# Performance work log

Hardware: AMD Instinct MI355X
Metric: run time of the kernel (lower is better)

## Reference

```python
import jax, jax.numpy as jnp
import numpy as np

B, C, H, W = 16, 16, 256, 256
HID, OUT_C, IN_C = 128, 13, 3

_SOBEL_X = np.array([[-1, 0, 1], [-2, 0, 2], [-1, 0, 1]], dtype=np.float32)
_SOBEL_Y = _SOBEL_X.T


def setup_inputs() -> dict:
    key = jax.random.key(0)
    k1, k2, k3, k4 = jax.random.split(key, 4)
    return {
        "input_grid": jax.random.normal(k1, (B, C, H, W), dtype=jnp.float32),
        "w1": jax.random.normal(k2, (HID, 3 * C), dtype=jnp.float32) * 0.0001,
        "b1": jax.random.normal(k3, (HID,), dtype=jnp.float32) * 0.0001,
        "w2": jax.random.normal(k4, (OUT_C, HID), dtype=jnp.float32) * 0.0001,
    }


def _depthwise_sobel(x_padded, filt2d):
    # x_padded: [B, C, H+2, W+2]; depthwise 3x3 valid conv (groups=C)
    c = x_padded.shape[1]
    kern = jnp.broadcast_to(jnp.asarray(filt2d)[None, None], (c, 1, 3, 3))
    return jax.lax.conv_general_dilated(
        x_padded, kern, window_strides=(1, 1), padding="VALID",
        feature_group_count=c,
        dimension_numbers=("NCHW", "OIHW", "NCHW"))


def reference(input_grid, w1, b1, w2):
    # circular pad by 1 on spatial dims
    xp = jnp.pad(input_grid, ((0, 0), (0, 0), (1, 1), (1, 1)), mode="wrap")
    gx = _depthwise_sobel(xp, _SOBEL_X)
    gy = _depthwise_sobel(xp, _SOBEL_Y)
    # perception grid: [B, 3C, H, W]
    perception = jnp.concatenate([input_grid, gx, gy], axis=1)
    # update network: 1x1 conv -> ReLU -> 1x1 conv (dropout = identity in eval)
    h = jax.nn.relu(jnp.einsum("bchw,oc->bohw", perception, w1)
                    + b1[None, :, None, None])
    ds = jnp.einsum("bchw,oc->bohw", h, w2)  # [B, C-IN_C, H, W]
    # residual add to channels 3: of the state
    return input_grid.at[:, IN_C:].add(ds)
```

## Files before the change

### kernel.cpp

```cpp
#include <hip/hip_runtime.h>

#define BB   16
#define CC   16
#define HH   256
#define WW   256
#define HID  128
#define OUTC 13

typedef short short8 __attribute__((ext_vector_type(8)));
typedef float floatx16 __attribute__((ext_vector_type(16)));

__device__ __forceinline__ unsigned short f2bf(float x) {
    unsigned int u = __float_as_uint(x);
    u += 0x7fffu + ((u >> 16) & 1u);
    return (unsigned short)(u >> 16);
}
__device__ __forceinline__ unsigned int pack2(float lo, float hi) {
    return (unsigned int)f2bf(lo) | ((unsigned int)f2bf(hi) << 16);
}

#define W1F_BYTES 36864
#define W2F_OFF   36864

__global__ __launch_bounds__(256) void gca_prep(
    const float* __restrict__ w1, const float* __restrict__ w2,
    unsigned char* __restrict__ ws)
{
    const int id = blockIdx.x * 256 + threadIdx.x;
    const float SX[9] = {-1.f, 0.f, 1.f, -2.f, 0.f, 2.f, -1.f, 0.f, 1.f};
    const float SY[9] = {-1.f, -2.f, -1.f, 0.f, 0.f, 0.f, 1.f, 2.f, 1.f};

    if (id < 2304) {
        const int mtG  = id / 576;
        const int rem  = id % 576;
        const int tap  = rem / 64;
        const int lane = rem % 64;
        const int p  = lane & 31, hi = lane >> 5;
        const int hid = 32 * mtG + p;
        const float cen = (tap == 4) ? 1.f : 0.f;
        const float sxv = SX[tap], syv = SY[tap];
        const float* wr = w1 + hid * 48;
        unsigned int o[4];
        for (int k = 0; k < 4; ++k) {
            int c0 = 8 * hi + 2 * k;
            float v0 = wr[c0]     * cen + wr[16 + c0]     * sxv + wr[32 + c0]     * syv;
            float v1 = wr[c0 + 1] * cen + wr[16 + c0 + 1] * sxv + wr[32 + c0 + 1] * syv;
            o[k] = (unsigned int)f2bf(v0) | ((unsigned int)f2bf(v1) << 16);
        }
        *(uint4*)(ws + (size_t)id * 16) = make_uint4(o[0], o[1], o[2], o[3]);
    } else if (id < 2816) {
        const int id2 = id - 2304;
        const int s    = id2 / 64;
        const int lane = id2 % 64;
        const int outc = lane & 31, hi = lane >> 5;
        unsigned int o[4];
        for (int k = 0; k < 4; ++k) {
            int hid0 = 16 * s + 8 * hi + 2 * k;
            float v0 = (outc < OUTC) ? w2[outc * HID + hid0]     : 0.f;
            float v1 = (outc < OUTC) ? w2[outc * HID + hid0 + 1] : 0.f;
            o[k] = (unsigned int)f2bf(v0) | ((unsigned int)f2bf(v1) << 16);
        }
        *(uint4*)(ws + W2F_OFF + (size_t)id2 * 16) = make_uint4(o[0], o[1], o[2], o[3]);
    }
}

#define TILE_DW 3400
#define CBUF_DW 1152
#define LDS_DW  (TILE_DW + CBUF_DW)

__global__ __launch_bounds__(128) void gca_main(
    const float* __restrict__ in,
    const float* __restrict__ b1,
    const unsigned char* __restrict__ ws,
    float* __restrict__ out)
{
    __shared__ unsigned int lds[LDS_DW];

    const int tid  = threadIdx.x;
    const int wid  = tid >> 6;
    const int lane = tid & 63;
    const int hw   = wid;
    const int p    = lane & 31;
    const int hi   = lane >> 5;

    const int bI = blockIdx.x >> 8;
    const int rm = blockIdx.x & 255;
    const int y0 = (rm >> 3) << 3;
    const int x0 = (rm & 7)  << 5;

    const float* inb  = in  + ((size_t)bI << 20);
    float*       outb = out + ((size_t)bI << 20);

    {
        const int g = tid >> 5, l = tid & 31;
        const float* cp0 = inb + ((size_t)(2 * g) << 16);
        const int xA = (x0 + l - 1) & 255;
        const int xB = (x0 + l + 31) & 255;
        const int ldsA = l * 10 + g;
        const int ldsB = (l + 32) * 10 + g;
        const bool doB = (l < 2);
        for (int rw = 0; rw < 10; ++rw) {
            const int yo = ((y0 + rw - 1) & 255) << 8;
            float a0 = cp0[yo + xA];
            float a1 = cp0[yo + xA + (1 << 16)];
            float b0 = cp0[yo + xA + (8 << 16)];
            float b1v = cp0[yo + xA + (9 << 16)];
            lds[rw * 340 + ldsA]     = pack2(a0, a1);
            lds[rw * 340 + ldsA + 4] = pack2(b0, b1v);
            if (doB) {
                float c0 = cp0[yo + xB];
                float c1 = cp0[yo + xB + (1 << 16)];
                float d0 = cp0[yo + xB + (8 << 16)];
                float d1 = cp0[yo + xB + (9 << 16)];
                lds[rw * 340 + ldsB]     = pack2(c0, c1);
                lds[rw * 340 + ldsB + 4] = pack2(d0, d1);
            }
        }
    }
    __syncthreads();

    const unsigned char* w1f = ws + ((size_t)(2 * hw) * 9) * 64 * 16;
    const unsigned char* w2f = ws + W2F_OFF + (size_t)(4 * hw) * 64 * 16;
    const int cb = TILE_DW + lane * 18;

#pragma unroll 1
    for (int t = 0; t < 8; ++t) {
        const int row = y0 + t;

        floatx16 acc1[2];
#pragma unroll
        for (int m = 0; m < 2; ++m) {
            const int hb = 64 * hw + 32 * m + 4 * hi;
#pragma unroll
            for (int rr = 0; rr < 4; ++rr) {
                float4 bv = *(const float4*)(b1 + hb + 8 * rr);
                acc1[m][4 * rr + 0] = bv.x;
                acc1[m][4 * rr + 1] = bv.y;
                acc1[m][4 * rr + 2] = bv.z;
                acc1[m][4 * rr + 3] = bv.w;
            }
        }

#pragma unroll
        for (int tap = 0; tap < 9; ++tap) {
            const int tr  = t + tap / 3;
            const int col = p + tap % 3;
            const int dwo = (tr * 34 + col) * 10 + 4 * hi;
            union { unsigned int u[4]; short8 s; } bfr;
            uint2 lo2 = *(const uint2*)&lds[dwo];
            uint2 hi2 = *(const uint2*)&lds[dwo + 2];
            bfr.u[0] = lo2.x; bfr.u[1] = lo2.y; bfr.u[2] = hi2.x; bfr.u[3] = hi2.y;
#pragma unroll
            for (int m = 0; m < 2; ++m) {
                short8 af = *(const short8*)(w1f + (size_t)((m * 9 + tap) * 64 + lane) * 16);
                acc1[m] = __builtin_amdgcn_mfma_f32_32x32x16_bf16(af, bfr.s, acc1[m], 0, 0, 0);
            }
        }

        uint2 hrun[8];
#pragma unroll
        for (int m = 0; m < 2; ++m)
#pragma unroll
            for (int rr = 0; rr < 4; ++rr) {
                float h0 = fmaxf(acc1[m][4 * rr + 0], 0.f);
                float h1 = fmaxf(acc1[m][4 * rr + 1], 0.f);
                float h2 = fmaxf(acc1[m][4 * rr + 2], 0.f);
                float h3 = fmaxf(acc1[m][4 * rr + 3], 0.f);
                hrun[4 * m + rr].x = pack2(h0, h1);
                hrun[4 * m + rr].y = pack2(h2, h3);
            }

        floatx16 acc2 = {};
#pragma unroll
        for (int sp = 0; sp < 4; ++sp) {
            uint2 r0 = hrun[2 * sp];
            uint2 r1 = hrun[2 * sp + 1];
            uint2 x0s, x1s;
            x0s.x = (unsigned int)__shfl_xor((int)r0.x, 32);
            x0s.y = (unsigned int)__shfl_xor((int)r0.y, 32);
            x1s.x = (unsigned int)__shfl_xor((int)r1.x, 32);
            x1s.y = (unsigned int)__shfl_xor((int)r1.y, 32);
            union { unsigned int u[4]; short8 s; } b2;
            uint2 lo = hi ? x1s : r0;
            uint2 hg = hi ? r1  : x0s;
            b2.u[0] = lo.x; b2.u[1] = lo.y; b2.u[2] = hg.x; b2.u[3] = hg.y;
            short8 a2 = *(const short8*)(w2f + (size_t)(sp * 64 + lane) * 16);
            acc2 = __builtin_amdgcn_mfma_f32_32x32x16_bf16(a2, b2.s, acc2, 0, 0, 0);
        }

        if (hw == 1) {
#pragma unroll
            for (int k = 0; k < 8; ++k) {
                uint2 v;
                v.x = __float_as_uint(acc2[2 * k]);
                v.y = __float_as_uint(acc2[2 * k + 1]);
                *(uint2*)&lds[cb + 2 * k] = v;
            }
        }
        __syncthreads();

        if (hw == 0) {
#pragma unroll
            for (int r = 0; r < 16; ++r) {
                int outc = (r & 3) + 8 * (r >> 2) + 4 * hi;
                if (outc < OUTC) {
                    float sum = acc2[r] + __uint_as_float(lds[cb + r]);
                    int idx = ((bI * 16 + 3 + outc) << 16) + (row << 8) + x0 + p;
                    out[idx] = in[idx] + sum;
                }
            }
        } else {
#pragma unroll
            for (int k = 0; k < 2; ++k) {
                int e = lane + 64 * k;
                if (e < 96) {
                    int c  = e >> 5;
                    int px = e & 31;
                    int idx = ((bI * 16 + c) << 16) + (row << 8) + x0 + px;
                    out[idx] = in[idx];
                }
            }
        }
        __syncthreads();
    }
}

extern "C" void kernel_launch(void* const* d_in, const int* in_sizes, int n_in,
                              void* d_out, int out_size, void* d_ws, size_t ws_size,
                              hipStream_t stream) {
    const float* x  = (const float*)d_in[0];
    const float* w1 = (const float*)d_in[1];
    const float* b1 = (const float*)d_in[2];
    const float* w2 = (const float*)d_in[3];
    float* out = (float*)d_out;
    unsigned char* ws = (unsigned char*)d_ws;

    hipLaunchKernelGGL(gca_prep, dim3(11), dim3(256), 0, stream, w1, w2, ws);
    hipLaunchKernelGGL(gca_main, dim3(4096), dim3(128), 0, stream, x, b1, ws, out);
}
```

Measured before the change: 248.9 us.

## Share hidden activations via LDS so both waves run full second GEMM

The hidden activations of both waves are now written to LDS as bf16, packed with the hardware v_cvt_pk_bf16_f32 instruction. Each wave then runs the full 128-deep second MFMA chain and keeps only alternating output rows, which replaces the partial-sum exchange through LDS. The residual input is prefetched before the first GEMM and placed in the accumulator, so the output store no longer needs the extra add and load. The channel copy is split across both waves, and launch bounds now request 4 blocks per SIMD. In exchange, each wave does twice the second-GEMM MFMA work, which is redundant, and the per-row barrier is moved rather than removed.

```diff
diff --git a/kernel.cpp b/kernel.cpp
--- a/kernel.cpp
+++ b/kernel.cpp
@@ -17,6 +17,11 @@
 }
 __device__ __forceinline__ unsigned int pack2(float lo, float hi) {
     return (unsigned int)f2bf(lo) | ((unsigned int)f2bf(hi) << 16);
+}
+__device__ __forceinline__ unsigned int cvt_pk_bf16(float lo, float hi) {
+    unsigned int d;
+    asm("v_cvt_pk_bf16_f32 %0, %1, %2" : "=v"(d) : "v"(lo), "v"(hi));
+    return d;
 }
 
 #define W1F_BYTES 36864
@@ -65,10 +70,10 @@
 }
 
 #define TILE_DW 3400
-#define CBUF_DW 1152
-#define LDS_DW  (TILE_DW + CBUF_DW)
-
-__global__ __launch_bounds__(128) void gca_main(
+#define H_DW    2048
+#define LDS_DW  (TILE_DW + H_DW)
+
+__global__ __launch_bounds__(128, 4) void gca_main(
     const float* __restrict__ in,
     const float* __restrict__ b1,
     const unsigned char* __restrict__ ws,
@@ -77,9 +82,8 @@
     __shared__ unsigned int lds[LDS_DW];
 
     const int tid  = threadIdx.x;
-    const int wid  = tid >> 6;
+    const int hw   = tid >> 6;
     const int lane = tid & 63;
-    const int hw   = wid;
     const int p    = lane & 31;
     const int hi   = lane >> 5;
 
@@ -120,12 +124,23 @@
     __syncthreads();
 
     const unsigned char* w1f = ws + ((size_t)(2 * hw) * 9) * 64 * 16;
-    const unsigned char* w2f = ws + W2F_OFF + (size_t)(4 * hw) * 64 * 16;
-    const int cb = TILE_DW + lane * 18;
+    const unsigned char* w2f = ws + W2F_OFF;
+
+    const int hwb = TILE_DW + (16 * hw + hi) * 64 + 2 * p;
+    const int hrb = TILE_DW + hi * 128 + 2 * p;
 
 #pragma unroll 1
     for (int t = 0; t < 8; ++t) {
-        const int row = y0 + t;
+        const int row   = y0 + t;
+        const int ibase = (row << 8) + x0 + p;
+
+        float rs[8];
+#pragma unroll
+        for (int j = 0; j < 8; ++j) {
+            const int r  = 2 * j + hw;
+            const int oc = (r & 3) + 8 * (r >> 2) + 4 * hi;
+            rs[j] = (oc < OUTC) ? inb[ibase + ((3 + oc) << 16)] : 0.f;
+        }
 
         floatx16 acc1[2];
 #pragma unroll
@@ -157,7 +172,6 @@
             }
         }
 
-        uint2 hrun[8];
 #pragma unroll
         for (int m = 0; m < 2; ++m)
 #pragma unroll
@@ -166,61 +180,58 @@
                 float h1 = fmaxf(acc1[m][4 * rr + 1], 0.f);
                 float h2 = fmaxf(acc1[m][4 * rr + 2], 0.f);
                 float h3 = fmaxf(acc1[m][4 * rr + 3], 0.f);
-                hrun[4 * m + rr].x = pack2(h0, h1);
-                hrun[4 * m + rr].y = pack2(h2, h3);
-            }
+                uint2 v;
+                v.x = cvt_pk_bf16(h0, h1);
+                v.y = cvt_pk_bf16(h2, h3);
+                *(uint2*)&lds[hwb + (8 * m + 2 * rr) * 64] = v;
+            }
+        __syncthreads();
 
         floatx16 acc2 = {};
-#pragma unroll
-        for (int sp = 0; sp < 4; ++sp) {
-            uint2 r0 = hrun[2 * sp];
-            uint2 r1 = hrun[2 * sp + 1];
-            uint2 x0s, x1s;
-            x0s.x = (unsigned int)__shfl_xor((int)r0.x, 32);
-            x0s.y = (unsigned int)__shfl_xor((int)r0.y, 32);
-            x1s.x = (unsigned int)__shfl_xor((int)r1.x, 32);
-            x1s.y = (unsigned int)__shfl_xor((int)r1.y, 32);
+        if (hw == 0) {
+            acc2[0]  = rs[0]; acc2[2]  = rs[1]; acc2[4]  = rs[2]; acc2[6]  = rs[3];
+            acc2[8]  = rs[4]; acc2[10] = rs[5]; acc2[12] = rs[6]; acc2[14] = rs[7];
+        } else {
+            acc2[1]  = rs[0]; acc2[3]  = rs[1]; acc2[5]  = rs[2]; acc2[7]  = rs[3];
+            acc2[9]  = rs[4]; acc2[11] = rs[5]; acc2[13] = rs[6]; acc2[15] = rs[7];
+        }
+
+#pragma unroll
+        for (int sp = 0; sp < 8; ++sp) {
+            uint2 u0 = *(const uint2*)&lds[hrb + sp * 256];
+            uint2 u1 = *(const uint2*)&lds[hrb + sp * 256 + 64];
             union { unsigned int u[4]; short8 s; } b2;
-            uint2 lo = hi ? x1s : r0;
-            uint2 hg = hi ? r1  : x0s;
-            b2.u[0] = lo.x; b2.u[1] = lo.y; b2.u[2] = hg.x; b2.u[3] = hg.y;
+            b2.u[0] = u0.x; b2.u[1] = u0.y; b2.u[2] = u1.x; b2.u[3] = u1.y;
             short8 a2 = *(const short8*)(w2f + (size_t)(sp * 64 + lane) * 16);
             acc2 = __builtin_amdgcn_mfma_f32_32x32x16_bf16(a2, b2.s, acc2, 0, 0, 0);
         }
 
-        if (hw == 1) {
-#pragma unroll
-            for (int k = 0; k < 8; ++k) {
-                uint2 v;
-                v.x = __float_as_uint(acc2[2 * k]);
-                v.y = __float_as_uint(acc2[2 * k + 1]);
-                *(uint2*)&lds[cb + 2 * k] = v;
-            }
-        }
-        __syncthreads();
-
         if (hw == 0) {
 #pragma unroll
-            for (int r = 0; r < 16; ++r) {
-                int outc = (r & 3) + 8 * (r >> 2) + 4 * hi;
-                if (outc < OUTC) {
-                    float sum = acc2[r] + __uint_as_float(lds[cb + r]);
-                    int idx = ((bI * 16 + 3 + outc) << 16) + (row << 8) + x0 + p;
-                    out[idx] = in[idx] + sum;
-                }
+            for (int j = 0; j < 8; ++j) {
+                const int r  = 2 * j;
+                const int oc = (r & 3) + 8 * (r >> 2) + 4 * hi;
+                if (oc < OUTC)
+                    outb[ibase + ((3 + oc) << 16)] = acc2[2 * j];
             }
         } else {
 #pragma unroll
-            for (int k = 0; k < 2; ++k) {
-                int e = lane + 64 * k;
-                if (e < 96) {
-                    int c  = e >> 5;
-                    int px = e & 31;
-                    int idx = ((bI * 16 + c) << 16) + (row << 8) + x0 + px;
-                    out[idx] = in[idx];
-                }
-            }
-        }
+            for (int j = 0; j < 8; ++j) {
+                const int r  = 2 * j + 1;
+                const int oc = (r & 3) + 8 * (r >> 2) + 4 * hi;
+                if (oc < OUTC)
+                    outb[ibase + ((3 + oc) << 16)] = acc2[2 * j + 1];
+            }
+        }
+
+        if (lane < 48) {
+            const int e  = 48 * hw + lane;
+            const int c  = e >> 5;
+            const int px = e & 31;
+            const int idx = (c << 16) + (row << 8) + x0 + px;
+            outb[idx] = inb[idx];
+        }
+
         __syncthreads();
     }
 }
```

After: 433.8 us. 74.3% more time.
